# Kernel tuning notes

Hardware: AMD Instinct MI355X
Metric: run time of the kernel (lower is better)

## Reference

```python
import jax, jax.numpy as jnp
import numpy as np

N_HEAD = 16
N_KV_HEAD = 4
HEAD_DIM = 64
ROPE_THETA = 10000.0
EPS = 1e-6


def _rope_cos_sin(T, D, theta):
    # matches torch: freqs_cis[t, i] = exp(1j * t * theta**(-2i/D)), i in [0, D//2)
    inv_freq = theta ** (-jnp.arange(0, D, 2, dtype=jnp.float32) / D)  # [D//2]
    freqs = jnp.arange(T, dtype=jnp.float32)[:, None] * inv_freq[None, :]  # [T, D//2]
    return jnp.cos(freqs), jnp.sin(freqs)


def _apply_rope(x, cos, sin):
    # x: [B, T, H, D]; pairs are (even, odd) along last dim, complex-multiplied by freqs_cis
    B, T, H, D = x.shape
    xr = x.reshape(B, T, H, D // 2, 2)
    xe, xo = xr[..., 0], xr[..., 1]
    c = cos[None, :, None, :]  # [1, T, 1, D//2]
    s = sin[None, :, None, :]
    oe = xe * c - xo * s
    oo = xe * s + xo * c
    return jnp.stack([oe, oo], axis=-1).reshape(B, T, H, D)


def _qk_norm(x):
    rms = jnp.sqrt(jnp.mean(x * x, axis=-1, keepdims=True) + EPS)
    return x / rms


def setup_inputs() -> dict:
    key = jax.random.key(0)
    k = jax.random.split(key, 5)
    B, T, C = 4, 2048, 1024
    sc = 1.0 / np.sqrt(C)
    return {
        "x": jax.random.normal(k[0], (B, T, C), jnp.float32),
        "wq": jax.random.normal(k[1], (N_HEAD * HEAD_DIM, C), jnp.float32) * sc,
        "wk": jax.random.normal(k[2], (N_KV_HEAD * HEAD_DIM, C), jnp.float32) * sc,
        "wv": jax.random.normal(k[3], (N_KV_HEAD * HEAD_DIM, C), jnp.float32) * sc,
        "wo": jax.random.normal(k[4], (C, N_HEAD * HEAD_DIM), jnp.float32) * sc,
    }


def reference(x, wq, wk, wv, wo):
    B, T, C = x.shape
    H, KVH, D = N_HEAD, N_KV_HEAD, HEAD_DIM
    n_rep = H // KVH

    q = (x @ wq.T).reshape(B, T, H, D)
    k = (x @ wk.T).reshape(B, T, KVH, D)
    v = (x @ wv.T).reshape(B, T, KVH, D)

    cos, sin = _rope_cos_sin(T, D, ROPE_THETA)
    q = _qk_norm(_apply_rope(q, cos, sin))
    k = _qk_norm(_apply_rope(k, cos, sin))

    # GQA expand kv heads to n_head
    k = jnp.repeat(k, n_rep, axis=2)  # [B, T, H, D]
    v = jnp.repeat(v, n_rep, axis=2)

    q = q.transpose(0, 2, 1, 3)  # [B, H, T, D]
    k = k.transpose(0, 2, 1, 3)
    v = v.transpose(0, 2, 1, 3)

    scale = 1.0 / np.sqrt(D)
    scores = jnp.einsum("bhqd,bhkd->bhqk", q, k) * scale
    causal = jnp.tril(jnp.ones((T, T), dtype=bool))
    scores = jnp.where(causal[None, None], scores, -jnp.inf)
    attn = jax.nn.softmax(scores, axis=-1)
    y = jnp.einsum("bhqk,bhkd->bhqd", attn, v)  # [B, H, T, D]
    y = y.transpose(0, 2, 1, 3).reshape(B, T, H * D)
    return y @ wo.T
```

## Files before the change

kernel.cpp:

```cpp
#include <hip/hip_runtime.h>
#include <hip/hip_bf16.h>
#include <type_traits>

typedef __attribute__((ext_vector_type(8))) __bf16 bf16x8;
typedef __attribute__((ext_vector_type(2))) float f32x2;
typedef __attribute__((ext_vector_type(4))) float f32x4;
typedef __attribute__((ext_vector_type(16))) float f32x16;

#define MFMA16(a, b, c) __builtin_amdgcn_mfma_f32_16x16x32_bf16((a), (b), (c), 0, 0, 0)
#define MFMA32(a, b, c) __builtin_amdgcn_mfma_f32_32x32x16_bf16((a), (b), (c), 0, 0, 0)

template <bool B> struct BoolC { static constexpr bool value = B; };

__device__ __forceinline__ unsigned short f2bf(float f) {
    unsigned u = __builtin_bit_cast(unsigned, f);
    u = (u + 0x7fffu + ((u >> 16) & 1u)) >> 16;
    return (unsigned short)u;
}

__device__ __forceinline__ float bf2f(unsigned short u) {
    return __builtin_bit_cast(float, (unsigned)u << 16);
}

__device__ __forceinline__ unsigned cvt_pk_bf16(float lo, float hi) {
    unsigned r;
    asm("v_cvt_pk_bf16_f32 %0, %1, %2" : "=v"(r) : "v"(lo), "v"(hi));
    return r;
}

__device__ __forceinline__ void permswap(unsigned& a, unsigned& b) {
    asm("v_permlane32_swap_b32 %0, %1" : "+v"(a), "+v"(b));
}

__device__ __forceinline__ void gll16(const void* g, void* l) {
    __builtin_amdgcn_global_load_lds((const __attribute__((address_space(1))) void*)g,
                                     (__attribute__((address_space(3))) void*)l, 16, 0, 0);
}

__global__ __launch_bounds__(256) void cvt_fused(const float4* __restrict__ x,
                                                 const float4* __restrict__ wq,
                                                 const float4* __restrict__ wk,
                                                 const float4* __restrict__ wv,
                                                 const float4* __restrict__ wo,
                                                 ushort4* __restrict__ xb,
                                                 ushort4* __restrict__ wqkvb,
                                                 ushort4* __restrict__ wob,
                                                 float2* __restrict__ tbl) {
    int i = blockIdx.x * 256 + threadIdx.x;
    if (i < 2752512) {
        const float4* src; ushort4* dst; int j;
        if (i < 2097152)      { src = x;  dst = xb;             j = i; }
        else if (i < 2359296) { src = wq; dst = wqkvb;          j = i - 2097152; }
        else if (i < 2424832) { src = wk; dst = wqkvb + 262144; j = i - 2359296; }
        else if (i < 2490368) { src = wv; dst = wqkvb + 327680; j = i - 2424832; }
        else                  { src = wo; dst = wob;            j = i - 2490368; }
        float4 v = src[j];
        ushort4 o;
        o.x = f2bf(v.x); o.y = f2bf(v.y); o.z = f2bf(v.z); o.w = f2bf(v.w);
        dst[j] = o;
    } else {
        int j = i - 2752512;
        int t = j >> 5, k = j & 31;
        float inv = powf(10000.0f, -(float)(2 * k) * (1.0f / 64.0f));
        float a = (float)t * inv;
        tbl[j] = make_float2(cosf(a), sinf(a));
    }
}

template <typename OT>
__global__ __launch_bounds__(256) void gemm_bt_t(const unsigned short* __restrict__ A,
                                                 const unsigned short* __restrict__ Bt,
                                                 OT* __restrict__ C, int M, int N, int K) {
    __shared__ unsigned short As[2][128 * 32];
    __shared__ unsigned short Bs[2][128 * 32];
    const int tid = threadIdx.x;
    const int wid = tid >> 6, lane = tid & 63;
    const size_t brow = (size_t)blockIdx.x * 128, bcol = (size_t)blockIdx.y * 128;
    const int nkt = K >> 5;

    auto stage = [&](int buf, int kt) {
#pragma unroll
        for (int j = 0; j < 2; ++j) {
            int e = (j * 256 + tid) * 8;
            int r = e >> 5, c = e & 31;
            gll16(A + (brow + r) * K + kt * 32 + c, &As[buf][e]);
        }
#pragma unroll
        for (int j = 0; j < 2; ++j) {
            int e = (j * 256 + tid) * 8;
            int r = e >> 5, c = e & 31;
            gll16(Bt + (bcol + r) * K + kt * 32 + c, &Bs[buf][e]);
        }
    };

    f32x4 acc[4][4] = {};
    const int wm = (wid >> 1) * 64, wn = (wid & 1) * 64;
    const int fr = lane & 15, fk = (lane >> 4) * 8;

    stage(0, 0);
    for (int kt = 0; kt < nkt; ++kt) {
        __syncthreads();
        if (kt + 1 < nkt) stage((kt + 1) & 1, kt + 1);
        const int buf = kt & 1;
        bf16x8 af[4], bfr[4];
#pragma unroll
        for (int i = 0; i < 4; ++i)
            af[i] = *(const bf16x8*)&As[buf][(wm + i * 16 + fr) * 32 + fk];
#pragma unroll
        for (int i = 0; i < 4; ++i)
            bfr[i] = *(const bf16x8*)&Bs[buf][(wn + i * 16 + fr) * 32 + fk];
#pragma unroll
        for (int i = 0; i < 4; ++i)
#pragma unroll
            for (int j = 0; j < 4; ++j)
                acc[i][j] = MFMA16(af[i], bfr[j], acc[i][j]);
    }

    const int orow = (lane >> 4) * 4, ocol = lane & 15;
#pragma unroll
    for (int i = 0; i < 4; ++i)
#pragma unroll
        for (int j = 0; j < 4; ++j)
#pragma unroll
            for (int r = 0; r < 4; ++r) {
                size_t idx = (brow + wm + i * 16 + orow + r) * N + (bcol + wn + j * 16 + ocol);
                if constexpr (std::is_same_v<OT, unsigned short>)
                    C[idx] = f2bf(acc[i][j][r]);
                else
                    C[idx] = acc[i][j][r];
            }
}

__global__ __launch_bounds__(256) void rope_norm(const unsigned short* __restrict__ qkvb,
                                                 const float2* __restrict__ tbl,
                                                 unsigned short* __restrict__ qb,
                                                 unsigned short* __restrict__ kb) {
    int unit = blockIdx.x * 4 + (threadIdx.x >> 6);
    int lane = threadIdx.x & 63;
    int row = unit / 20;
    int hh = unit - row * 20;
    int b = row >> 11, t = row & 2047;
    int col = (hh < 16) ? hh * 64 : 1024 + (hh - 16) * 64;
    float x = bf2f(qkvb[(size_t)row * 1536 + col + lane]);
    float partner = __shfl_xor(x, 1);
    float2 cs = tbl[t * 32 + (lane >> 1)];
    float sgn = (lane & 1) ? cs.y : -cs.y;
    float o = x * cs.x + partner * sgn;
    float ss = o * o;
#pragma unroll
    for (int off = 1; off < 64; off <<= 1) ss += __shfl_xor(ss, off);
    o = o * rsqrtf(ss * (1.0f / 64.0f) + 1e-6f);
    if (hh < 16) o *= 0.18033688f;
    unsigned short ob = f2bf(o);
    if (hh < 16)
        qb[(((size_t)(b * 16 + hh)) * 2048 + t) * 64 + lane] = ob;
    else
        kb[(((size_t)(b * 4 + (hh - 16))) * 2048 + t) * 64 + lane] = ob;
}

__global__ __launch_bounds__(256) void vtrans(const unsigned short* __restrict__ qkvb,
                                              unsigned short* __restrict__ vt) {
    __shared__ unsigned short tile[64][72];
    int bk = blockIdx.y, t0 = blockIdx.x * 64;
    int b = bk >> 2, kvh = bk & 3;
    int i = threadIdx.x >> 2, c0 = (threadIdx.x & 3) * 16;
    const unsigned short* src = qkvb + ((size_t)(b * 2048 + t0)) * 1536 + 1280 + kvh * 64;
#pragma unroll
    for (int j = 0; j < 16; ++j) tile[i][c0 + j] = src[(size_t)i * 1536 + c0 + j];
    __syncthreads();
    unsigned short* dst = vt + (size_t)bk * 64 * 2048 + (size_t)i * 2048 + t0 + c0;
#pragma unroll
    for (int j = 0; j < 16; ++j) dst[j] = tile[c0 + j][i];
}

__global__ __launch_bounds__(256) void attn_fwd(const unsigned short* __restrict__ qb,
                                                const unsigned short* __restrict__ kbuf,
                                                const unsigned short* __restrict__ vt,
                                                float* __restrict__ accOg,
                                                float* __restrict__ accLg) {
    int orig = blockIdx.x;
    int wg = (orig & 7) * 320 + (orig >> 3);
    int bh = wg / 40;
    int u = 39 - (wg - bh * 40);
    int qt, ci, nc;
    if (u < 4)       { qt = u;               ci = 0;            nc = 1; }
    else if (u < 12) { qt = 4 + ((u - 4) >> 1);  ci = (u - 4) & 1;  nc = 2; }
    else if (u < 24) { qt = 8 + (u - 12) / 3;    ci = (u - 12) % 3; nc = 3; }
    else             { qt = 12 + ((u - 24) >> 2); ci = (u - 24) & 3; nc = 4; }
    const int nkt = 2 * qt + 2;
    const int t0 = ci * nkt / nc, t1 = (ci + 1) * nkt / nc;
    const int qbase = qt * 128;

    int b = bh >> 4, h = bh & 15, kvh = h >> 2;
    int tid = threadIdx.x, wid = tid >> 6, lane = tid & 63;
    int qrow0 = qbase + wid * 32;
    const unsigned short* Q = qb + ((size_t)(b * 16 + h)) * 2048 * 64;
    const unsigned short* Kp = kbuf + ((size_t)(b * 4 + kvh)) * 2048 * 64;
    const unsigned short* Vp = vt + ((size_t)(b * 4 + kvh)) * 64 * 2048;
    const int q32 = lane & 31, hi = lane >> 5;
    const int swz = (q32 & 7) ^ ((q32 >> 3) & 3);

    __shared__ unsigned short Klds[3][4096];
    __shared__ unsigned short Vlds[3][4096];

    auto stage = [&](int buf, int kt) {
#pragma unroll
        for (int j = 0; j < 2; ++j) {
            int t = j * 256 + tid;
            int k = t >> 3, c = (t & 7) ^ (k & 7) ^ ((k >> 3) & 3);
            gll16(Kp + ((size_t)(kt * 64 + k)) * 64 + c * 8, &Klds[buf][t * 8]);
        }
#pragma unroll
        for (int j = 0; j < 2; ++j) {
            int t = j * 256 + tid;
            int d = t >> 3, c = (t & 7) ^ (d & 7) ^ ((d >> 3) & 3);
            gll16(Vp + (size_t)d * 2048 + kt * 64 + c * 8, &Vlds[buf][t * 8]);
        }
    };

    bf16x8 qf[4];
#pragma unroll
    for (int kd = 0; kd < 4; ++kd)
        qf[kd] = *(const bf16x8*)&Q[(qrow0 + q32) * 64 + kd * 16 + hi * 8];

    f32x16 accO[2] = {};
    f32x2 lr2 = {0.0f, 0.0f};
    f32x16 s0v;
#pragma unroll
    for (int i = 0; i < 16; ++i) s0v[i] = -11.54156036f;

    const int nt = t1 - t0;
    stage(0, t0);
    if (nt > 1) stage(1, t0 + 1);
    int cur = 0;
    for (int kt = t0; kt < t1; ++kt) {
        if (kt + 1 < t1) { asm volatile("s_waitcnt vmcnt(4)" ::: "memory"); }
        else             { asm volatile("s_waitcnt vmcnt(0)" ::: "memory"); }
        __builtin_amdgcn_sched_barrier(0);
        __builtin_amdgcn_s_barrier();
        if (kt + 2 < t1) stage(cur == 0 ? 2 : cur - 1, kt + 2);
        const int kb0 = kt * 64;
        if (kb0 <= qrow0 + 31) {
            f32x16 s[2] = {s0v, s0v};
            __builtin_amdgcn_s_setprio(1);
#pragma unroll
            for (int j = 0; j < 2; ++j) {
                int row = j * 32 + q32;
#pragma unroll
                for (int kd = 0; kd < 4; ++kd) {
                    bf16x8 kf = *(const bf16x8*)&Klds[cur][row * 64 + ((2 * kd + hi) ^ swz) * 8];
                    s[j] = MFMA32(kf, qf[kd], s[j]);
                }
            }
            __builtin_amdgcn_s_setprio(0);
            const int qg = qrow0 + q32;
            bf16x8 pf[4];
            auto build = [&](auto mc) {
                constexpr bool MASKED = decltype(mc)::value;
#pragma unroll
                for (int j = 0; j < 2; ++j) {
                    float p[16];
#pragma unroll
                    for (int r = 0; r < 16; ++r) {
                        float v = __builtin_exp2f(s[j][r]);
                        if (MASKED) {
                            int key = kb0 + j * 32 + (r & 3) + 8 * (r >> 2) + 4 * hi;
                            if (key > qg) v = 0.0f;
                        }
                        p[r] = v;
                    }
#pragma unroll
                    for (int i = 0; i < 8; ++i) {
                        f32x2 pp = {p[2 * i], p[2 * i + 1]};
                        asm("v_pk_add_f32 %0, %0, %1" : "+v"(lr2) : "v"(pp));
                    }
#pragma unroll
                    for (int kl = 0; kl < 2; ++kl) {
                        unsigned c0 = cvt_pk_bf16(p[8 * kl + 0], p[8 * kl + 1]);
                        unsigned c1 = cvt_pk_bf16(p[8 * kl + 4], p[8 * kl + 5]);
                        unsigned c2 = cvt_pk_bf16(p[8 * kl + 2], p[8 * kl + 3]);
                        unsigned c3 = cvt_pk_bf16(p[8 * kl + 6], p[8 * kl + 7]);
                        permswap(c0, c1);
                        permswap(c2, c3);
                        union { bf16x8 v; unsigned u[4]; } pk;
                        pk.u[0] = c0; pk.u[1] = c2; pk.u[2] = c1; pk.u[3] = c3;
                        pf[j * 2 + kl] = pk.v;
                    }
                }
            };
            if (kb0 + 63 > qrow0) build(BoolC<true>{});
            else                  build(BoolC<false>{});
            __builtin_amdgcn_s_setprio(1);
#pragma unroll
            for (int nd = 0; nd < 2; ++nd) {
                int row = nd * 32 + q32;
#pragma unroll
                for (int ks = 0; ks < 4; ++ks) {
                    bf16x8 vf = *(const bf16x8*)&Vlds[cur][row * 64 + ((2 * ks + hi) ^ swz) * 8];
                    accO[nd] = MFMA32(pf[ks], vf, accO[nd]);
                }
            }
            __builtin_amdgcn_s_setprio(0);
        }
        cur = (cur == 2) ? 0 : cur + 1;
    }

    float lrun = lr2[0] + lr2[1];
    unsigned lu = __builtin_bit_cast(unsigned, lrun);
    unsigned la = lu, lb = lu;
    permswap(la, lb);
    float L = __builtin_bit_cast(float, la) + __builtin_bit_cast(float, lb);

    if (t0 * 64 <= qrow0 + 31) {
#pragma unroll
        for (int nd = 0; nd < 2; ++nd)
#pragma unroll
            for (int r = 0; r < 16; ++r) {
                int rowq = qrow0 + (r & 3) + 8 * (r >> 2) + 4 * hi;
                atomicAdd(accOg + ((size_t)bh * 2048 + rowq) * 64 + nd * 32 + q32, accO[nd][r]);
            }
        if (lane < 32) atomicAdd(accLg + (size_t)bh * 2048 + qrow0 + q32, L);
    }
}

__global__ __launch_bounds__(256) void attn_fin(const float* __restrict__ accOg,
                                                const float* __restrict__ accLg,
                                                unsigned short* __restrict__ y) {
    int idx = blockIdx.x * 256 + threadIdx.x;
    int dg = idx & 15;
    int row = idx >> 4;
    int bh = row >> 11, t = row & 2047;
    int b = bh >> 4, h = bh & 15;
    f32x4 o = *(const f32x4*)&accOg[(size_t)row * 64 + dg * 4];
    float inv = 1.0f / accLg[row];
    ushort4 w;
    w.x = f2bf(o[0] * inv); w.y = f2bf(o[1] * inv);
    w.z = f2bf(o[2] * inv); w.w = f2bf(o[3] * inv);
    *(ushort4*)&y[((size_t)(b * 2048 + t)) * 1024 + h * 64 + dg * 4] = w;
}

extern "C" void kernel_launch(void* const* d_in, const int* in_sizes, int n_in,
                              void* d_out, int out_size, void* d_ws, size_t ws_size,
                              hipStream_t stream) {
    const float* x = (const float*)d_in[0];
    const float* wq = (const float*)d_in[1];
    const float* wk = (const float*)d_in[2];
    const float* wv = (const float*)d_in[3];
    const float* wo = (const float*)d_in[4];
    float* out = (float*)d_out;

    char* ws = (char*)d_ws;
    size_t off = 0;
    auto alloc = [&](size_t bytes) {
        void* p = ws + off;
        off += (bytes + 255) & ~(size_t)255;
        return p;
    };
    unsigned short* xb    = (unsigned short*)alloc(8192ull * 1024 * 2);
    unsigned short* wqkvb = (unsigned short*)alloc(1536ull * 1024 * 2);
    unsigned short* wob   = (unsigned short*)alloc(1024ull * 1024 * 2);
    char*           big   = (char*)alloc((64ull * 2048 * 64 + 64ull * 2048) * 4);
    float2*         tbl   = (float2*)alloc(2048ull * 32 * 8);
    unsigned short* qb    = (unsigned short*)alloc(8192ull * 1024 * 2);
    unsigned short* kb    = (unsigned short*)alloc(4ull * 4 * 2048 * 64 * 2);
    unsigned short* vt    = (unsigned short*)alloc(4ull * 4 * 64 * 2048 * 2);

    unsigned short* qkvb  = (unsigned short*)big;
    float*          accO  = (float*)big;
    float*          accL  = accO + 64ull * 2048 * 64;
    unsigned short* ybf   = xb;

    cvt_fused<<<11008, 256, 0, stream>>>((const float4*)x, (const float4*)wq, (const float4*)wk,
                                         (const float4*)wv, (const float4*)wo,
                                         (ushort4*)xb, (ushort4*)wqkvb, (ushort4*)wob, tbl);

    gemm_bt_t<unsigned short><<<dim3(64, 12), 256, 0, stream>>>(xb, wqkvb, qkvb, 8192, 1536, 1024);

    rope_norm<<<(8192 * 20) / 4, 256, 0, stream>>>(qkvb, tbl, qb, kb);

    vtrans<<<dim3(32, 16), 256, 0, stream>>>(qkvb, vt);

    hipMemsetAsync(accO, 0, (64ull * 2048 * 64 + 64ull * 2048) * 4, stream);

    attn_fwd<<<2560, 256, 0, stream>>>(qb, kb, vt, accO, accL);

    attn_fin<<<8192, 256, 0, stream>>>(accO, accL, ybf);

    gemm_bt_t<float><<<dim3(64, 8), 256, 0, stream>>>(ybf, wob, out, 8192, 1024, 1024);
}
```

Baseline: 203.7 us.

## Replace atomic split-K attention reduction with per-chunk bf16 partials reduced in finalize

The attention kernel no longer atomically adds fp32 partial outputs and row sums into a zeroed buffer. Each split chunk now writes its own bf16 partial output and fp32 row sum to a dedicated slot, and the finalize kernel sums the one to four chunks per query tile before normalizing. This removes the memset and the atomic traffic. In exchange, partials are rounded to bf16 before summation, and because the partials carry no per-chunk max, this relies on the chunks sharing a common scaling.

```diff
diff --git a/kernel.cpp b/kernel.cpp
--- a/kernel.cpp
+++ b/kernel.cpp
@@ -176,8 +176,8 @@
 __global__ __launch_bounds__(256) void attn_fwd(const unsigned short* __restrict__ qb,
                                                 const unsigned short* __restrict__ kbuf,
                                                 const unsigned short* __restrict__ vt,
-                                                float* __restrict__ accOg,
-                                                float* __restrict__ accLg) {
+                                                unsigned short* __restrict__ Pp,
+                                                float* __restrict__ Lp) {
     int orig = blockIdx.x;
     int wg = (orig & 7) * 320 + (orig >> 3);
     int bh = wg / 40;
@@ -311,31 +311,43 @@
     permswap(la, lb);
     float L = __builtin_bit_cast(float, la) + __builtin_bit_cast(float, lb);
 
-    if (t0 * 64 <= qrow0 + 31) {
-#pragma unroll
-        for (int nd = 0; nd < 2; ++nd)
-#pragma unroll
-            for (int r = 0; r < 16; ++r) {
-                int rowq = qrow0 + (r & 3) + 8 * (r >> 2) + 4 * hi;
-                atomicAdd(accOg + ((size_t)bh * 2048 + rowq) * 64 + nd * 32 + q32, accO[nd][r]);
-            }
-        if (lane < 32) atomicAdd(accLg + (size_t)bh * 2048 + qrow0 + q32, L);
-    }
-}
-
-__global__ __launch_bounds__(256) void attn_fin(const float* __restrict__ accOg,
-                                                const float* __restrict__ accLg,
+    unsigned short* Pw = Pp + (((size_t)bh * 40 + u) * 128 + wid * 32) * 64;
+#pragma unroll
+    for (int nd = 0; nd < 2; ++nd)
+#pragma unroll
+        for (int r = 0; r < 16; ++r) {
+            int lrow = (r & 3) + 8 * (r >> 2) + 4 * hi;
+            Pw[(size_t)lrow * 64 + nd * 32 + q32] = f2bf(accO[nd][r]);
+        }
+    if (lane < 32)
+        Lp[((size_t)bh * 40 + u) * 128 + wid * 32 + q32] = L;
+}
+
+__global__ __launch_bounds__(256) void attn_fin(const unsigned short* __restrict__ Pp,
+                                                const float* __restrict__ Lp,
                                                 unsigned short* __restrict__ y) {
     int idx = blockIdx.x * 256 + threadIdx.x;
     int dg = idx & 15;
-    int row = idx >> 4;
-    int bh = row >> 11, t = row & 2047;
+    int grow = idx >> 4;
+    int bh = grow >> 11, t = grow & 2047;
     int b = bh >> 4, h = bh & 15;
-    f32x4 o = *(const f32x4*)&accOg[(size_t)row * 64 + dg * 4];
-    float inv = 1.0f / accLg[row];
+    int qt = t >> 7;
+    int bse, nc;
+    if (qt < 4)       { bse = qt;                nc = 1; }
+    else if (qt < 8)  { bse = 4 + 2 * (qt - 4);  nc = 2; }
+    else if (qt < 12) { bse = 12 + 3 * (qt - 8); nc = 3; }
+    else              { bse = 24 + 4 * (qt - 12); nc = 4; }
+    float o0 = 0.f, o1 = 0.f, o2 = 0.f, o3 = 0.f, L = 0.f;
+    for (int ci = 0; ci < nc; ++ci) {
+        size_t slot = ((size_t)bh * 40 + bse + ci) * 128 + (t & 127);
+        ushort4 pw = *(const ushort4*)&Pp[slot * 64 + dg * 4];
+        o0 += bf2f(pw.x); o1 += bf2f(pw.y); o2 += bf2f(pw.z); o3 += bf2f(pw.w);
+        L += Lp[slot];
+    }
+    float inv = 1.0f / L;
     ushort4 w;
-    w.x = f2bf(o[0] * inv); w.y = f2bf(o[1] * inv);
-    w.z = f2bf(o[2] * inv); w.w = f2bf(o[3] * inv);
+    w.x = f2bf(o0 * inv); w.y = f2bf(o1 * inv);
+    w.z = f2bf(o2 * inv); w.w = f2bf(o3 * inv);
     *(ushort4*)&y[((size_t)(b * 2048 + t)) * 1024 + h * 64 + dg * 4] = w;
 }
 
@@ -359,15 +371,15 @@
     unsigned short* xb    = (unsigned short*)alloc(8192ull * 1024 * 2);
     unsigned short* wqkvb = (unsigned short*)alloc(1536ull * 1024 * 2);
     unsigned short* wob   = (unsigned short*)alloc(1024ull * 1024 * 2);
-    char*           big   = (char*)alloc((64ull * 2048 * 64 + 64ull * 2048) * 4);
+    char*           big   = (char*)alloc(41943040ull + 1310720ull);
     float2*         tbl   = (float2*)alloc(2048ull * 32 * 8);
     unsigned short* qb    = (unsigned short*)alloc(8192ull * 1024 * 2);
     unsigned short* kb    = (unsigned short*)alloc(4ull * 4 * 2048 * 64 * 2);
     unsigned short* vt    = (unsigned short*)alloc(4ull * 4 * 64 * 2048 * 2);
 
     unsigned short* qkvb  = (unsigned short*)big;
-    float*          accO  = (float*)big;
-    float*          accL  = accO + 64ull * 2048 * 64;
+    unsigned short* Pp    = (unsigned short*)big;
+    float*          Lp    = (float*)(big + 41943040ull);
     unsigned short* ybf   = xb;
 
     cvt_fused<<<11008, 256, 0, stream>>>((const float4*)x, (const float4*)wq, (const float4*)wk,
@@ -380,11 +392,9 @@
 
     vtrans<<<dim3(32, 16), 256, 0, stream>>>(qkvb, vt);
 
-    hipMemsetAsync(accO, 0, (64ull * 2048 * 64 + 64ull * 2048) * 4, stream);
-
-    attn_fwd<<<2560, 256, 0, stream>>>(qb, kb, vt, accO, accL);
-
-    attn_fin<<<8192, 256, 0, stream>>>(accO, accL, ybf);
+    attn_fwd<<<2560, 256, 0, stream>>>(qb, kb, vt, Pp, Lp);
+
+    attn_fin<<<8192, 256, 0, stream>>>(Pp, Lp, ybf);
 
     gemm_bt_t<float><<<dim3(64, 8), 256, 0, stream>>>(ybf, wob, out, 8192, 1024, 1024);
 }
```

Result: faster. 188.6 us (-7.5%).
